# Kernel optimization log

Measured on AMD Instinct MI355X. Metric: run time of the kernel, lower is better.

## Reference

```python
import jax, jax.numpy as jnp
import numpy as np

NEG_BIG = -1e12
ALPHA = 0.2  # leaky_relu negative slope


def setup_inputs() -> dict:
    key = jax.random.key(0)
    k1, k2, k3, k4, k5 = jax.random.split(key, 5)
    B, N, C_in, C_out = 8, 2048, 128, 128
    x = jax.random.normal(k1, (B, N, C_in), dtype=jnp.float32)
    adj = jax.random.randint(k2, (B, N, N), 0, 2, dtype=jnp.int32)
    W = jax.random.normal(k3, (C_in, C_out), dtype=jnp.float32)
    a = jax.random.normal(k4, (C_out, 2), dtype=jnp.float32)
    bias = jax.random.normal(k5, (C_out,), dtype=jnp.float32)
    return {"x": x, "adj": adj, "W": W, "a": a, "bias": bias}


def reference(x, adj, W, a, bias):
    # hidden: [B, N, C_out]
    hidden = jnp.matmul(x, W)
    # additive attention components: [B, N, 2] -> attn1, attn2 each [B, N]
    scores = jnp.matmul(hidden, a)
    attn1 = scores[..., 0]
    attn2 = scores[..., 1]
    # outer-sum: [B, N, N]
    attn = attn1[:, :, None] + attn2[:, None, :]
    attn = jnp.where(attn >= 0, attn, ALPHA * attn)  # leaky_relu
    attn = attn + jnp.where(adj > 0, 0.0, NEG_BIG)
    attn = jax.nn.softmax(attn, axis=-1)
    # dropout is identity in eval/reference mode
    out = jnp.matmul(attn, hidden) + bias
    return out
```

## Files before the change

kernel.cpp:

```cpp
#include <hip/hip_runtime.h>
#include <hip/hip_bf16.h>

#define ALPHA 0.2f
#define NEG_BIG -1e12f

constexpr int B_ = 8, N_ = 2048, C_ = 128;
constexpr int IB = 16, JB = 128, NJT = N_ / JB;

typedef __attribute__((ext_vector_type(8))) short short8;
typedef __attribute__((ext_vector_type(8))) unsigned short ushort8;
typedef __attribute__((ext_vector_type(4))) float f32x4;

__device__ __forceinline__ unsigned short f2bf(float f) {
    unsigned int u = __float_as_uint(f);
    u += 0x7fffu + ((u >> 16) & 1u);
    return (unsigned short)(u >> 16);
}

__device__ __forceinline__ unsigned int cvtpk_bf16(float lo, float hi) {
    unsigned int r;
    asm("v_cvt_pk_bf16_f32 %0, %1, %2" : "=v"(r) : "v"(lo), "v"(hi));
    return r;
}

__device__ __forceinline__ void barrier_lds_only() {
    asm volatile("s_waitcnt lgkmcnt(0)" ::: "memory");
    __builtin_amdgcn_s_barrier();
}

__global__ __launch_bounds__(256) void k1_hidden(
    const float* __restrict__ x, const float* __restrict__ W,
    const float* __restrict__ a, unsigned short* __restrict__ hT,
    float* __restrict__ at1, float* __restrict__ at2)
{
    __shared__ float xs[64][C_];
    __shared__ float Ws[C_][C_];
    const int tid = threadIdx.x;
    const int row0 = blockIdx.x * 64;

    {
        const float4* xsrc = (const float4*)(x + (size_t)row0 * C_);
        float4* xdst = (float4*)&xs[0][0];
        for (int i = tid; i < 64 * C_ / 4; i += 256) xdst[i] = xsrc[i];
        const float4* wsrc = (const float4*)W;
        float4* wdst = (float4*)&Ws[0][0];
        for (int i = tid; i < C_ * C_ / 4; i += 256) wdst[i] = wsrc[i];
    }
    __syncthreads();

    const int tr = tid >> 5, tc = tid & 31;
    const int r0 = tr * 8, c0 = tc * 4;

    float acc[8][4];
#pragma unroll
    for (int i = 0; i < 8; ++i)
#pragma unroll
        for (int j = 0; j < 4; ++j) acc[i][j] = 0.f;

    for (int k = 0; k < C_; k += 4) {
        float4 w0 = *(const float4*)&Ws[k + 0][c0];
        float4 w1 = *(const float4*)&Ws[k + 1][c0];
        float4 w2 = *(const float4*)&Ws[k + 2][c0];
        float4 w3 = *(const float4*)&Ws[k + 3][c0];
#pragma unroll
        for (int rr = 0; rr < 8; ++rr) {
            float4 xv = *(const float4*)&xs[r0 + rr][k];
            acc[rr][0] += xv.x * w0.x + xv.y * w1.x + xv.z * w2.x + xv.w * w3.x;
            acc[rr][1] += xv.x * w0.y + xv.y * w1.y + xv.z * w2.y + xv.w * w3.y;
            acc[rr][2] += xv.x * w0.z + xv.y * w1.z + xv.z * w2.z + xv.w * w3.z;
            acc[rr][3] += xv.x * w0.w + xv.y * w1.w + xv.z * w2.w + xv.w * w3.w;
        }
    }

    float av0[4], av1[4];
#pragma unroll
    for (int cc = 0; cc < 4; ++cc) {
        av0[cc] = a[(c0 + cc) * 2 + 0];
        av1[cc] = a[(c0 + cc) * 2 + 1];
    }
#pragma unroll
    for (int rr = 0; rr < 8; ++rr) {
        float s1 = acc[rr][0] * av0[0] + acc[rr][1] * av0[1] +
                   acc[rr][2] * av0[2] + acc[rr][3] * av0[3];
        float s2 = acc[rr][0] * av1[0] + acc[rr][1] * av1[1] +
                   acc[rr][2] * av1[2] + acc[rr][3] * av1[3];
#pragma unroll
        for (int off = 1; off < 32; off <<= 1) {
            s1 += __shfl_xor(s1, off);
            s2 += __shfl_xor(s2, off);
        }
        if (tc == 0) {
            at1[row0 + r0 + rr] = s1;
            at2[row0 + r0 + rr] = s2;
        }
    }

    const int b = row0 >> 11;
    const int n0 = row0 & (N_ - 1);
#pragma unroll
    for (int cc = 0; cc < 4; ++cc) {
        ushort8 hv;
#pragma unroll
        for (int rr = 0; rr < 8; ++rr) hv[rr] = f2bf(acc[rr][cc]);
        *(ushort8*)(hT + ((size_t)b * C_ + c0 + cc) * N_ + n0 + r0) = hv;
    }
}

__global__ __launch_bounds__(256, 4) void k2_attn(
    const int* __restrict__ adj, const unsigned short* __restrict__ hT,
    const float* __restrict__ at1, const float* __restrict__ at2,
    const float* __restrict__ bias, float* __restrict__ out)
{
    __shared__ unsigned short P[2][IB][JB + 8];
    __shared__ float at2s[N_];
    __shared__ float mrow[IB], lrow[IB], srow[2][IB];

    const int tid = threadIdx.x;
    const int b  = blockIdx.x >> 7;
    const int i0 = (blockIdx.x & 127) * IB;

    {
        const float4* src = (const float4*)(at2 + (size_t)b * N_);
        float4* dst = (float4*)at2s;
        dst[tid]       = src[tid];
        dst[tid + 256] = src[tid + 256];
    }
    if (tid < IB) { mrow[tid] = -3e38f; lrow[tid] = 0.f; }

    const int r  = tid >> 4;
    const int jl = tid & 15;
    const float a1 = at1[(size_t)b * N_ + i0 + r];
    const int* arow = adj + ((size_t)(b * N_ + i0 + r)) * N_ + jl * 8;

    const int lane = tid & 63;
    const int wv = tid >> 6;
    const int lg = lane >> 4;
    const int ll = lane & 15;
    const unsigned short* hb = hT + ((size_t)b * C_ + wv * 32 + ll) * N_;

    f32x4 acc0 = {0.f, 0.f, 0.f, 0.f}, acc1 = {0.f, 0.f, 0.f, 0.f};

    __syncthreads();

    int4 pf0 = *(const int4*)arow;
    int4 pf1 = *(const int4*)(arow + 4);

    for (int jt = 0; jt < NJT; ++jt) {
        const int buf = jt & 1;

        short8 vb0[4], vb1[4];
        {
            const unsigned short* hrow = hb + jt * JB + lg * 8;
#pragma unroll
            for (int ks = 0; ks < 4; ++ks) {
                vb0[ks] = *(const short8*)(hrow + ks * 32);
                vb1[ks] = *(const short8*)(hrow + (size_t)16 * N_ + ks * 32);
            }
        }

        int4 A0 = pf0, A1 = pf1;
        if (jt + 1 < NJT) {
            pf0 = *(const int4*)(arow + (jt + 1) * JB);
            pf1 = *(const int4*)(arow + (jt + 1) * JB + 4);
        }
        float4 f0 = *(const float4*)&at2s[jt * JB + jl * 8];
        float4 f1 = *(const float4*)&at2s[jt * JB + jl * 8 + 4];

        float s[8];
        {
            float t;
            t = a1 + f0.x; t = fmaxf(t, ALPHA * t); s[0] = A0.x > 0 ? t : NEG_BIG;
            t = a1 + f0.y; t = fmaxf(t, ALPHA * t); s[1] = A0.y > 0 ? t : NEG_BIG;
            t = a1 + f0.z; t = fmaxf(t, ALPHA * t); s[2] = A0.z > 0 ? t : NEG_BIG;
            t = a1 + f0.w; t = fmaxf(t, ALPHA * t); s[3] = A0.w > 0 ? t : NEG_BIG;
            t = a1 + f1.x; t = fmaxf(t, ALPHA * t); s[4] = A1.x > 0 ? t : NEG_BIG;
            t = a1 + f1.y; t = fmaxf(t, ALPHA * t); s[5] = A1.y > 0 ? t : NEG_BIG;
            t = a1 + f1.z; t = fmaxf(t, ALPHA * t); s[6] = A1.z > 0 ? t : NEG_BIG;
            t = a1 + f1.w; t = fmaxf(t, ALPHA * t); s[7] = A1.w > 0 ? t : NEG_BIG;
        }
        float tm = fmaxf(fmaxf(fmaxf(s[0], s[1]), fmaxf(s[2], s[3])),
                         fmaxf(fmaxf(s[4], s[5]), fmaxf(s[6], s[7])));
        tm = fmaxf(tm, __shfl_xor(tm, 1));
        tm = fmaxf(tm, __shfl_xor(tm, 2));
        tm = fmaxf(tm, __shfl_xor(tm, 4));
        tm = fmaxf(tm, __shfl_xor(tm, 8));

        const float m_old = mrow[r];
        const float m_new = fmaxf(m_old, tm);

        float p[8];
        float ps = 0.f;
#pragma unroll
        for (int e = 0; e < 8; ++e) { p[e] = __expf(s[e] - m_new); ps += p[e]; }
        ps += __shfl_xor(ps, 1);
        ps += __shfl_xor(ps, 2);
        ps += __shfl_xor(ps, 4);
        ps += __shfl_xor(ps, 8);

        int4 pw;
        pw.x = (int)cvtpk_bf16(p[0], p[1]);
        pw.y = (int)cvtpk_bf16(p[2], p[3]);
        pw.z = (int)cvtpk_bf16(p[4], p[5]);
        pw.w = (int)cvtpk_bf16(p[6], p[7]);
        *(int4*)&P[buf][r][jl * 8] = pw;

        if (jl == 0) {
            const float sc = __expf(m_old - m_new);
            srow[buf][r] = sc;
            mrow[r] = m_new;
            lrow[r] = lrow[r] * sc + ps;
        }
        barrier_lds_only();

        const char* Pb = (const char*)P[buf];
        short8 pa[4];
#pragma unroll
        for (int ks = 0; ks < 4; ++ks)
            pa[ks] = *(const short8*)(Pb + ll * 272 + ks * 64 + lg * 16);

        float4 sc4 = *(const float4*)&srow[buf][lg * 4];
        acc0[0] *= sc4.x; acc0[1] *= sc4.y; acc0[2] *= sc4.z; acc0[3] *= sc4.w;
        acc1[0] *= sc4.x; acc1[1] *= sc4.y; acc1[2] *= sc4.z; acc1[3] *= sc4.w;

        __builtin_amdgcn_s_setprio(1);
#pragma unroll
        for (int ks = 0; ks < 4; ++ks) {
            acc0 = __builtin_amdgcn_mfma_f32_16x16x32_bf16(pa[ks], vb0[ks], acc0, 0, 0, 0);
            acc1 = __builtin_amdgcn_mfma_f32_16x16x32_bf16(pa[ks], vb1[ks], acc1, 0, 0, 0);
        }
        __builtin_amdgcn_s_setprio(0);
    }

    float4 lw = *(const float4*)&lrow[lg * 4];
    const int c = wv * 32 + ll;
    const float bv0 = bias[c];
    const float bv1 = bias[c + 16];

    float* o = out + ((size_t)(b * N_ + i0 + lg * 4)) * C_ + c;
    o[0 * C_]      = acc0[0] / lw.x + bv0;
    o[1 * C_]      = acc0[1] / lw.y + bv0;
    o[2 * C_]      = acc0[2] / lw.z + bv0;
    o[3 * C_]      = acc0[3] / lw.w + bv0;
    o[0 * C_ + 16] = acc1[0] / lw.x + bv1;
    o[1 * C_ + 16] = acc1[1] / lw.y + bv1;
    o[2 * C_ + 16] = acc1[2] / lw.z + bv1;
    o[3 * C_ + 16] = acc1[3] / lw.w + bv1;
}

extern "C" void kernel_launch(void* const* d_in, const int* in_sizes, int n_in,
                              void* d_out, int out_size, void* d_ws, size_t ws_size,
                              hipStream_t stream) {
    const float* x    = (const float*)d_in[0];
    const int*   adj  = (const int*)d_in[1];
    const float* W    = (const float*)d_in[2];
    const float* a    = (const float*)d_in[3];
    const float* bias = (const float*)d_in[4];
    float* out = (float*)d_out;

    char* ws = (char*)d_ws;
    unsigned short* hT = (unsigned short*)ws;
    float* at1 = (float*)(ws + (size_t)4 * 1024 * 1024);
    float* at2 = (float*)(ws + (size_t)4 * 1024 * 1024 + 64 * 1024);

    k1_hidden<<<(B_ * N_) / 64, 256, 0, stream>>>(x, W, a, hT, at1, at2);
    k2_attn<<<B_ * (N_ / IB), 256, 0, stream>>>(adj, hT, at1, at2, bias, out);
}
```

Before: 86.93 us.

## Compute softmax probabilities in MFMA operand layout to eliminate LDS staging and barriers

The attention kernel is restructured so that each wave computes the 16x128 probability tile itself, already laid out as the MFMA B operand, and multiplies it against transposed hidden tiles as the A operand. The shared P buffer, per-row max/sum arrays and the per-tile barrier go away, and row statistics stay in registers through cross-lane shuffles. Blocks shrink to 128 threads (two waves, each covering 64 output channels) and each thread loads a whole adjacency row tile. Each wave now recomputes the full score and exp work for the tile, so that work is duplicated across waves, and register pressure rises with 32 probabilities and a double-buffered adjacency prefetch.

```diff
diff --git a/kernel.cpp b/kernel.cpp
--- a/kernel.cpp
+++ b/kernel.cpp
@@ -5,7 +5,7 @@
 #define NEG_BIG -1e12f
 
 constexpr int B_ = 8, N_ = 2048, C_ = 128;
-constexpr int IB = 16, JB = 128, NJT = N_ / JB;
+constexpr int JB = 128, NJT = N_ / JB;
 
 typedef __attribute__((ext_vector_type(8))) short short8;
 typedef __attribute__((ext_vector_type(8))) unsigned short ushort8;
@@ -21,11 +21,6 @@
     unsigned int r;
     asm("v_cvt_pk_bf16_f32 %0, %1, %2" : "=v"(r) : "v"(lo), "v"(hi));
     return r;
-}
-
-__device__ __forceinline__ void barrier_lds_only() {
-    asm volatile("s_waitcnt lgkmcnt(0)" ::: "memory");
-    __builtin_amdgcn_s_barrier();
 }
 
 __global__ __launch_bounds__(256) void k1_hidden(
@@ -106,145 +101,151 @@
     }
 }
 
-__global__ __launch_bounds__(256, 4) void k2_attn(
+__global__ __launch_bounds__(128, 2) void k2_attn(
     const int* __restrict__ adj, const unsigned short* __restrict__ hT,
     const float* __restrict__ at1, const float* __restrict__ at2,
     const float* __restrict__ bias, float* __restrict__ out)
 {
-    __shared__ unsigned short P[2][IB][JB + 8];
     __shared__ float at2s[N_];
-    __shared__ float mrow[IB], lrow[IB], srow[2][IB];
-
     const int tid = threadIdx.x;
     const int b  = blockIdx.x >> 7;
-    const int i0 = (blockIdx.x & 127) * IB;
+    const int i0 = (blockIdx.x & 127) * 16;
 
     {
         const float4* src = (const float4*)(at2 + (size_t)b * N_);
         float4* dst = (float4*)at2s;
-        dst[tid]       = src[tid];
-        dst[tid + 256] = src[tid + 256];
-    }
-    if (tid < IB) { mrow[tid] = -3e38f; lrow[tid] = 0.f; }
-
-    const int r  = tid >> 4;
-    const int jl = tid & 15;
-    const float a1 = at1[(size_t)b * N_ + i0 + r];
-    const int* arow = adj + ((size_t)(b * N_ + i0 + r)) * N_ + jl * 8;
+#pragma unroll
+        for (int k = 0; k < 4; ++k) dst[tid + 128 * k] = src[tid + 128 * k];
+    }
 
     const int lane = tid & 63;
     const int wv = tid >> 6;
-    const int lg = lane >> 4;
-    const int ll = lane & 15;
-    const unsigned short* hb = hT + ((size_t)b * C_ + wv * 32 + ll) * N_;
-
-    f32x4 acc0 = {0.f, 0.f, 0.f, 0.f}, acc1 = {0.f, 0.f, 0.f, 0.f};
+    const int r  = lane & 15;
+    const int jc = lane >> 4;
+
+    const float a1v = at1[(size_t)b * N_ + i0 + r];
+    const int* arow = adj + ((size_t)(b * N_ + i0 + r)) * N_ + jc * 8;
+    const unsigned short* hrow = hT + ((size_t)b * C_ + wv * 64 + r) * N_ + jc * 8;
+
+    f32x4 acc[4];
+#pragma unroll
+    for (int cb = 0; cb < 4; ++cb) acc[cb] = (f32x4){0.f, 0.f, 0.f, 0.f};
+    float m = -3e38f, l = 0.f;
+
+    int4 A[8];
+#pragma unroll
+    for (int q = 0; q < 8; ++q)
+        A[q] = *(const int4*)(arow + (q >> 1) * 32 + (q & 1) * 4);
 
     __syncthreads();
 
-    int4 pf0 = *(const int4*)arow;
-    int4 pf1 = *(const int4*)(arow + 4);
-
     for (int jt = 0; jt < NJT; ++jt) {
-        const int buf = jt & 1;
-
-        short8 vb0[4], vb1[4];
-        {
-            const unsigned short* hrow = hb + jt * JB + lg * 8;
-#pragma unroll
-            for (int ks = 0; ks < 4; ++ks) {
-                vb0[ks] = *(const short8*)(hrow + ks * 32);
-                vb1[ks] = *(const short8*)(hrow + (size_t)16 * N_ + ks * 32);
-            }
-        }
-
-        int4 A0 = pf0, A1 = pf1;
-        if (jt + 1 < NJT) {
-            pf0 = *(const int4*)(arow + (jt + 1) * JB);
-            pf1 = *(const int4*)(arow + (jt + 1) * JB + 4);
-        }
-        float4 f0 = *(const float4*)&at2s[jt * JB + jl * 8];
-        float4 f1 = *(const float4*)&at2s[jt * JB + jl * 8 + 4];
-
-        float s[8];
-        {
+        const int jn = (jt + 1 < NJT ? jt + 1 : jt) * JB;
+        int4 An[8];
+#pragma unroll
+        for (int q = 0; q < 8; ++q)
+            An[q] = *(const int4*)(arow + jn + (q >> 1) * 32 + (q & 1) * 4);
+
+        short8 h0[4], h1[4];
+#pragma unroll
+        for (int ks = 0; ks < 4; ++ks) {
+            h0[ks] = *(const short8*)(hrow + jt * JB + ks * 32);
+            h1[ks] = *(const short8*)(hrow + (size_t)16 * N_ + jt * JB + ks * 32);
+        }
+
+        float4 F[8];
+#pragma unroll
+        for (int q = 0; q < 8; ++q)
+            F[q] = *(const float4*)&at2s[jt * JB + (q >> 1) * 32 + jc * 8 + (q & 1) * 4];
+
+        float p[32];
+#pragma unroll
+        for (int q = 0; q < 8; ++q) {
             float t;
-            t = a1 + f0.x; t = fmaxf(t, ALPHA * t); s[0] = A0.x > 0 ? t : NEG_BIG;
-            t = a1 + f0.y; t = fmaxf(t, ALPHA * t); s[1] = A0.y > 0 ? t : NEG_BIG;
-            t = a1 + f0.z; t = fmaxf(t, ALPHA * t); s[2] = A0.z > 0 ? t : NEG_BIG;
-            t = a1 + f0.w; t = fmaxf(t, ALPHA * t); s[3] = A0.w > 0 ? t : NEG_BIG;
-            t = a1 + f1.x; t = fmaxf(t, ALPHA * t); s[4] = A1.x > 0 ? t : NEG_BIG;
-            t = a1 + f1.y; t = fmaxf(t, ALPHA * t); s[5] = A1.y > 0 ? t : NEG_BIG;
-            t = a1 + f1.z; t = fmaxf(t, ALPHA * t); s[6] = A1.z > 0 ? t : NEG_BIG;
-            t = a1 + f1.w; t = fmaxf(t, ALPHA * t); s[7] = A1.w > 0 ? t : NEG_BIG;
-        }
-        float tm = fmaxf(fmaxf(fmaxf(s[0], s[1]), fmaxf(s[2], s[3])),
-                         fmaxf(fmaxf(s[4], s[5]), fmaxf(s[6], s[7])));
-        tm = fmaxf(tm, __shfl_xor(tm, 1));
-        tm = fmaxf(tm, __shfl_xor(tm, 2));
-        tm = fmaxf(tm, __shfl_xor(tm, 4));
-        tm = fmaxf(tm, __shfl_xor(tm, 8));
-
-        const float m_old = mrow[r];
-        const float m_new = fmaxf(m_old, tm);
-
-        float p[8];
-        float ps = 0.f;
-#pragma unroll
-        for (int e = 0; e < 8; ++e) { p[e] = __expf(s[e] - m_new); ps += p[e]; }
-        ps += __shfl_xor(ps, 1);
-        ps += __shfl_xor(ps, 2);
-        ps += __shfl_xor(ps, 4);
-        ps += __shfl_xor(ps, 8);
-
-        int4 pw;
-        pw.x = (int)cvtpk_bf16(p[0], p[1]);
-        pw.y = (int)cvtpk_bf16(p[2], p[3]);
-        pw.z = (int)cvtpk_bf16(p[4], p[5]);
-        pw.w = (int)cvtpk_bf16(p[6], p[7]);
-        *(int4*)&P[buf][r][jl * 8] = pw;
-
-        if (jl == 0) {
-            const float sc = __expf(m_old - m_new);
-            srow[buf][r] = sc;
-            mrow[r] = m_new;
-            lrow[r] = lrow[r] * sc + ps;
-        }
-        barrier_lds_only();
-
-        const char* Pb = (const char*)P[buf];
-        short8 pa[4];
-#pragma unroll
-        for (int ks = 0; ks < 4; ++ks)
-            pa[ks] = *(const short8*)(Pb + ll * 272 + ks * 64 + lg * 16);
-
-        float4 sc4 = *(const float4*)&srow[buf][lg * 4];
-        acc0[0] *= sc4.x; acc0[1] *= sc4.y; acc0[2] *= sc4.z; acc0[3] *= sc4.w;
-        acc1[0] *= sc4.x; acc1[1] *= sc4.y; acc1[2] *= sc4.z; acc1[3] *= sc4.w;
-
+            t = a1v + F[q].x; t = fmaxf(t, ALPHA * t); p[q * 4 + 0] = A[q].x > 0 ? t : NEG_BIG;
+            t = a1v + F[q].y; t = fmaxf(t, ALPHA * t); p[q * 4 + 1] = A[q].y > 0 ? t : NEG_BIG;
+            t = a1v + F[q].z; t = fmaxf(t, ALPHA * t); p[q * 4 + 2] = A[q].z > 0 ? t : NEG_BIG;
+            t = a1v + F[q].w; t = fmaxf(t, ALPHA * t); p[q * 4 + 3] = A[q].w > 0 ? t : NEG_BIG;
+        }
+
+        short8 h2[4], h3[4];
+#pragma unroll
+        for (int ks = 0; ks < 4; ++ks) {
+            h2[ks] = *(const short8*)(hrow + (size_t)32 * N_ + jt * JB + ks * 32);
+            h3[ks] = *(const short8*)(hrow + (size_t)48 * N_ + jt * JB + ks * 32);
+        }
+
+        float u[16];
+#pragma unroll
+        for (int q = 0; q < 16; ++q) u[q] = fmaxf(p[q], p[q + 16]);
+#pragma unroll
+        for (int q = 0; q < 8; ++q) u[q] = fmaxf(u[q], u[q + 8]);
+#pragma unroll
+        for (int q = 0; q < 4; ++q) u[q] = fmaxf(u[q], u[q + 4]);
+        float tm = fmaxf(fmaxf(u[0], u[1]), fmaxf(u[2], u[3]));
+        tm = fmaxf(tm, __shfl_xor(tm, 16));
+        tm = fmaxf(tm, __shfl_xor(tm, 32));
+
+        const float m_new = fmaxf(m, tm);
+        const float sc = __expf(m - m_new);
+        m = m_new;
+
+#pragma unroll
+        for (int q = 0; q < 32; ++q) p[q] = __expf(p[q] - m_new);
+
+        float v[16];
+#pragma unroll
+        for (int q = 0; q < 16; ++q) v[q] = p[q] + p[q + 16];
+#pragma unroll
+        for (int q = 0; q < 8; ++q) v[q] = v[q] + v[q + 8];
+#pragma unroll
+        for (int q = 0; q < 4; ++q) v[q] = v[q] + v[q + 4];
+        float ps = (v[0] + v[1]) + (v[2] + v[3]);
+        ps += __shfl_xor(ps, 16);
+        ps += __shfl_xor(ps, 32);
+        l = l * sc + ps;
+
+        short8 Pb[4];
+#pragma unroll
+        for (int ks = 0; ks < 4; ++ks) {
+            int4 w;
+            w.x = (int)cvtpk_bf16(p[ks * 8 + 0], p[ks * 8 + 1]);
+            w.y = (int)cvtpk_bf16(p[ks * 8 + 2], p[ks * 8 + 3]);
+            w.z = (int)cvtpk_bf16(p[ks * 8 + 4], p[ks * 8 + 5]);
+            w.w = (int)cvtpk_bf16(p[ks * 8 + 6], p[ks * 8 + 7]);
+            Pb[ks] = *(short8*)&w;
+        }
+
+#pragma unroll
+        for (int cb = 0; cb < 4; ++cb) {
+            acc[cb][0] *= sc; acc[cb][1] *= sc; acc[cb][2] *= sc; acc[cb][3] *= sc;
+        }
         __builtin_amdgcn_s_setprio(1);
 #pragma unroll
         for (int ks = 0; ks < 4; ++ks) {
-            acc0 = __builtin_amdgcn_mfma_f32_16x16x32_bf16(pa[ks], vb0[ks], acc0, 0, 0, 0);
-            acc1 = __builtin_amdgcn_mfma_f32_16x16x32_bf16(pa[ks], vb1[ks], acc1, 0, 0, 0);
+            acc[0] = __builtin_amdgcn_mfma_f32_16x16x32_bf16(h0[ks], Pb[ks], acc[0], 0, 0, 0);
+            acc[1] = __builtin_amdgcn_mfma_f32_16x16x32_bf16(h1[ks], Pb[ks], acc[1], 0, 0, 0);
+            acc[2] = __builtin_amdgcn_mfma_f32_16x16x32_bf16(h2[ks], Pb[ks], acc[2], 0, 0, 0);
+            acc[3] = __builtin_amdgcn_mfma_f32_16x16x32_bf16(h3[ks], Pb[ks], acc[3], 0, 0, 0);
         }
         __builtin_amdgcn_s_setprio(0);
-    }
-
-    float4 lw = *(const float4*)&lrow[lg * 4];
-    const int c = wv * 32 + ll;
-    const float bv0 = bias[c];
-    const float bv1 = bias[c + 16];
-
-    float* o = out + ((size_t)(b * N_ + i0 + lg * 4)) * C_ + c;
-    o[0 * C_]      = acc0[0] / lw.x + bv0;
-    o[1 * C_]      = acc0[1] / lw.y + bv0;
-    o[2 * C_]      = acc0[2] / lw.z + bv0;
-    o[3 * C_]      = acc0[3] / lw.w + bv0;
-    o[0 * C_ + 16] = acc1[0] / lw.x + bv1;
-    o[1 * C_ + 16] = acc1[1] / lw.y + bv1;
-    o[2 * C_ + 16] = acc1[2] / lw.z + bv1;
-    o[3 * C_ + 16] = acc1[3] / lw.w + bv1;
+
+#pragma unroll
+        for (int q = 0; q < 8; ++q) A[q] = An[q];
+    }
+
+    const float invl = 1.f / l;
+#pragma unroll
+    for (int cb = 0; cb < 4; ++cb) {
+        const int c0 = wv * 64 + cb * 16 + jc * 4;
+        float4 bv = *(const float4*)&bias[c0];
+        float4 o;
+        o.x = acc[cb][0] * invl + bv.x;
+        o.y = acc[cb][1] * invl + bv.y;
+        o.z = acc[cb][2] * invl + bv.z;
+        o.w = acc[cb][3] * invl + bv.w;
+        *(float4*)(out + ((size_t)(b * N_ + i0 + r)) * C_ + c0) = o;
+    }
 }
 
 extern "C" void kernel_launch(void* const* d_in, const int* in_sizes, int n_in,
@@ -263,5 +264,5 @@
     float* at2 = (float*)(ws + (size_t)4 * 1024 * 1024 + 64 * 1024);
 
     k1_hidden<<<(B_ * N_) / 64, 256, 0, stream>>>(x, W, a, hT, at1, at2);
-    k2_attn<<<B_ * (N_ / IB), 256, 0, stream>>>(adj, hT, at1, at2, bias, out);
-}
+    k2_attn<<<B_ * (N_ / 16), 128, 0, stream>>>(adj, hT, at1, at2, bias, out);
+}
```

After: 113.0 us, median of 4. 1.3x slower.

## Pre-pack adjacency into bitmask and use exp2 with log2e-scaled scores

Applied to the files above, without the earlier changes.

Adds a streaming kernel that compresses the int32 adjacency matrix into one bit per entry, so the attention kernel reads a small bitmask instead of full int32 rows inside its softmax loop. The attention scores are pre-scaled by log2(e) in the hidden kernel so the softmax can use exp2 instead of exp. The full adjacency is still read once, but now by a simple bandwidth-oriented kernel. The cost is an extra launch and extra workspace writes, and the new 4 MB workspace region shifts the other buffers.

```diff
diff --git a/kernel.cpp b/kernel.cpp
--- a/kernel.cpp
+++ b/kernel.cpp
@@ -3,6 +3,7 @@
 
 #define ALPHA 0.2f
 #define NEG_BIG -1e12f
+#define LOG2E 1.44269504088896340736f
 
 constexpr int B_ = 8, N_ = 2048, C_ = 128;
 constexpr int IB = 16, JB = 128, NJT = N_ / JB;
@@ -26,6 +27,25 @@
 __device__ __forceinline__ void barrier_lds_only() {
     asm volatile("s_waitcnt lgkmcnt(0)" ::: "memory");
     __builtin_amdgcn_s_barrier();
+}
+
+__global__ __launch_bounds__(256) void k_pack(
+    const int* __restrict__ adj, unsigned int* __restrict__ abits)
+{
+    const size_t w = (size_t)blockIdx.x * 256 + threadIdx.x;
+    const int4* src = (const int4*)adj + w * 8;
+    int4 v[8];
+#pragma unroll
+    for (int q = 0; q < 8; ++q) v[q] = src[q];
+    unsigned int m = 0;
+#pragma unroll
+    for (int q = 0; q < 8; ++q) {
+        m |= (v[q].x > 0 ? 1u : 0u) << (q * 4 + 0);
+        m |= (v[q].y > 0 ? 1u : 0u) << (q * 4 + 1);
+        m |= (v[q].z > 0 ? 1u : 0u) << (q * 4 + 2);
+        m |= (v[q].w > 0 ? 1u : 0u) << (q * 4 + 3);
+    }
+    abits[w] = m;
 }
 
 __global__ __launch_bounds__(256) void k1_hidden(
@@ -90,8 +110,8 @@
             s2 += __shfl_xor(s2, off);
         }
         if (tc == 0) {
-            at1[row0 + r0 + rr] = s1;
-            at2[row0 + r0 + rr] = s2;
+            at1[row0 + r0 + rr] = s1 * LOG2E;
+            at2[row0 + r0 + rr] = s2 * LOG2E;
         }
     }
 
@@ -107,7 +127,7 @@
 }
 
 __global__ __launch_bounds__(256, 4) void k2_attn(
-    const int* __restrict__ adj, const unsigned short* __restrict__ hT,
+    const unsigned int* __restrict__ abits, const unsigned short* __restrict__ hT,
     const float* __restrict__ at1, const float* __restrict__ at2,
     const float* __restrict__ bias, float* __restrict__ out)
 {
@@ -129,8 +149,10 @@
 
     const int r  = tid >> 4;
     const int jl = tid & 15;
-    const float a1 = at1[(size_t)b * N_ + i0 + r];
-    const int* arow = adj + ((size_t)(b * N_ + i0 + r)) * N_ + jl * 8;
+    const float a1v = at1[(size_t)b * N_ + i0 + r];
+    const unsigned int* abrow =
+        abits + ((size_t)(b * N_ + i0 + r)) * (N_ / 32) + (jl >> 2);
+    const int sh = (jl & 3) * 8;
 
     const int lane = tid & 63;
     const int wv = tid >> 6;
@@ -142,11 +164,10 @@
 
     __syncthreads();
 
-    int4 pf0 = *(const int4*)arow;
-    int4 pf1 = *(const int4*)(arow + 4);
-
     for (int jt = 0; jt < NJT; ++jt) {
         const int buf = jt & 1;
+
+        const unsigned int wbits = abrow[jt * 4] >> sh;
 
         short8 vb0[4], vb1[4];
         {
@@ -158,25 +179,20 @@
             }
         }
 
-        int4 A0 = pf0, A1 = pf1;
-        if (jt + 1 < NJT) {
-            pf0 = *(const int4*)(arow + (jt + 1) * JB);
-            pf1 = *(const int4*)(arow + (jt + 1) * JB + 4);
-        }
         float4 f0 = *(const float4*)&at2s[jt * JB + jl * 8];
         float4 f1 = *(const float4*)&at2s[jt * JB + jl * 8 + 4];
 
         float s[8];
         {
             float t;
-            t = a1 + f0.x; t = fmaxf(t, ALPHA * t); s[0] = A0.x > 0 ? t : NEG_BIG;
-            t = a1 + f0.y; t = fmaxf(t, ALPHA * t); s[1] = A0.y > 0 ? t : NEG_BIG;
-            t = a1 + f0.z; t = fmaxf(t, ALPHA * t); s[2] = A0.z > 0 ? t : NEG_BIG;
-            t = a1 + f0.w; t = fmaxf(t, ALPHA * t); s[3] = A0.w > 0 ? t : NEG_BIG;
-            t = a1 + f1.x; t = fmaxf(t, ALPHA * t); s[4] = A1.x > 0 ? t : NEG_BIG;
-            t = a1 + f1.y; t = fmaxf(t, ALPHA * t); s[5] = A1.y > 0 ? t : NEG_BIG;
-            t = a1 + f1.z; t = fmaxf(t, ALPHA * t); s[6] = A1.z > 0 ? t : NEG_BIG;
-            t = a1 + f1.w; t = fmaxf(t, ALPHA * t); s[7] = A1.w > 0 ? t : NEG_BIG;
+            t = a1v + f0.x; t = fmaxf(t, ALPHA * t); s[0] = (wbits & 1u)   ? t : NEG_BIG;
+            t = a1v + f0.y; t = fmaxf(t, ALPHA * t); s[1] = (wbits & 2u)   ? t : NEG_BIG;
+            t = a1v + f0.z; t = fmaxf(t, ALPHA * t); s[2] = (wbits & 4u)   ? t : NEG_BIG;
+            t = a1v + f0.w; t = fmaxf(t, ALPHA * t); s[3] = (wbits & 8u)   ? t : NEG_BIG;
+            t = a1v + f1.x; t = fmaxf(t, ALPHA * t); s[4] = (wbits & 16u)  ? t : NEG_BIG;
+            t = a1v + f1.y; t = fmaxf(t, ALPHA * t); s[5] = (wbits & 32u)  ? t : NEG_BIG;
+            t = a1v + f1.z; t = fmaxf(t, ALPHA * t); s[6] = (wbits & 64u)  ? t : NEG_BIG;
+            t = a1v + f1.w; t = fmaxf(t, ALPHA * t); s[7] = (wbits & 128u) ? t : NEG_BIG;
         }
         float tm = fmaxf(fmaxf(fmaxf(s[0], s[1]), fmaxf(s[2], s[3])),
                          fmaxf(fmaxf(s[4], s[5]), fmaxf(s[6], s[7])));
@@ -191,7 +207,7 @@
         float p[8];
         float ps = 0.f;
 #pragma unroll
-        for (int e = 0; e < 8; ++e) { p[e] = __expf(s[e] - m_new); ps += p[e]; }
+        for (int e = 0; e < 8; ++e) { p[e] = exp2f(s[e] - m_new); ps += p[e]; }
         ps += __shfl_xor(ps, 1);
         ps += __shfl_xor(ps, 2);
         ps += __shfl_xor(ps, 4);
@@ -205,7 +221,7 @@
         *(int4*)&P[buf][r][jl * 8] = pw;
 
         if (jl == 0) {
-            const float sc = __expf(m_old - m_new);
+            const float sc = exp2f(m_old - m_new);
             srow[buf][r] = sc;
             mrow[r] = m_new;
             lrow[r] = lrow[r] * sc + ps;
@@ -258,10 +274,12 @@
     float* out = (float*)d_out;
 
     char* ws = (char*)d_ws;
-    unsigned short* hT = (unsigned short*)ws;
-    float* at1 = (float*)(ws + (size_t)4 * 1024 * 1024);
-    float* at2 = (float*)(ws + (size_t)4 * 1024 * 1024 + 64 * 1024);
-
+    unsigned int*   abits = (unsigned int*)ws;
+    unsigned short* hT  = (unsigned short*)(ws + (size_t)4 * 1024 * 1024);
+    float* at1 = (float*)(ws + (size_t)8 * 1024 * 1024);
+    float* at2 = (float*)(ws + (size_t)8 * 1024 * 1024 + 64 * 1024);
+
+    k_pack<<<(B_ * N_ * (N_ / 32)) / 256, 256, 0, stream>>>(adj, abits);
     k1_hidden<<<(B_ * N_) / 64, 256, 0, stream>>>(x, W, a, hT, at1, at2);
-    k2_attn<<<B_ * (N_ / IB), 256, 0, stream>>>(adj, hT, at1, at2, bias, out);
-}
+    k2_attn<<<B_ * (N_ / IB), 256, 0, stream>>>(abits, hT, at1, at2, bias, out);
+}
```

After: 106.6 us. 22.6% more time.

## Double attention row block to 32 rows and use exp2 with prescaled scores

Applied to the files above, without the earlier changes.

The attention kernel now handles 32 query rows per block with 512 threads, so two row-halves of waves share the same hT column tiles and at2 staging. This halves redundant loads of the bf16 hidden matrix per output row. The attention scores are also prescaled by log2(e) in the first kernel so the softmax can use exp2 instead of exp. In exchange the grid has half as many blocks, which may reduce load balance across CUs.

```diff
diff --git a/kernel.cpp b/kernel.cpp
--- a/kernel.cpp
+++ b/kernel.cpp
@@ -3,9 +3,10 @@
 
 #define ALPHA 0.2f
 #define NEG_BIG -1e12f
+#define LOG2E 1.44269504088896340736f
 
 constexpr int B_ = 8, N_ = 2048, C_ = 128;
-constexpr int IB = 16, JB = 128, NJT = N_ / JB;
+constexpr int IB = 32, JB = 128, NJT = N_ / JB;
 
 typedef __attribute__((ext_vector_type(8))) short short8;
 typedef __attribute__((ext_vector_type(8))) unsigned short ushort8;
@@ -90,8 +91,8 @@
             s2 += __shfl_xor(s2, off);
         }
         if (tc == 0) {
-            at1[row0 + r0 + rr] = s1;
-            at2[row0 + r0 + rr] = s2;
+            at1[row0 + r0 + rr] = s1 * LOG2E;
+            at2[row0 + r0 + rr] = s2 * LOG2E;
         }
     }
 
@@ -106,7 +107,7 @@
     }
 }
 
-__global__ __launch_bounds__(256, 4) void k2_attn(
+__global__ __launch_bounds__(512, 2) void k2_attn(
     const int* __restrict__ adj, const unsigned short* __restrict__ hT,
     const float* __restrict__ at1, const float* __restrict__ at2,
     const float* __restrict__ bias, float* __restrict__ out)
@@ -116,24 +117,21 @@
     __shared__ float mrow[IB], lrow[IB], srow[2][IB];
 
     const int tid = threadIdx.x;
-    const int b  = blockIdx.x >> 7;
-    const int i0 = (blockIdx.x & 127) * IB;
-
-    {
-        const float4* src = (const float4*)(at2 + (size_t)b * N_);
-        float4* dst = (float4*)at2s;
-        dst[tid]       = src[tid];
-        dst[tid + 256] = src[tid + 256];
-    }
+    const int b  = blockIdx.x >> 6;
+    const int i0 = (blockIdx.x & 63) * IB;
+
+    ((float4*)at2s)[tid] = ((const float4*)(at2 + (size_t)b * N_))[tid];
     if (tid < IB) { mrow[tid] = -3e38f; lrow[tid] = 0.f; }
 
     const int r  = tid >> 4;
     const int jl = tid & 15;
-    const float a1 = at1[(size_t)b * N_ + i0 + r];
+    const float a1v = at1[(size_t)b * N_ + i0 + r];
     const int* arow = adj + ((size_t)(b * N_ + i0 + r)) * N_ + jl * 8;
 
     const int lane = tid & 63;
-    const int wv = tid >> 6;
+    const int w  = tid >> 6;
+    const int wv = w & 3;
+    const int rh = w >> 2;
     const int lg = lane >> 4;
     const int ll = lane & 15;
     const unsigned short* hb = hT + ((size_t)b * C_ + wv * 32 + ll) * N_;
@@ -169,14 +167,14 @@
         float s[8];
         {
             float t;
-            t = a1 + f0.x; t = fmaxf(t, ALPHA * t); s[0] = A0.x > 0 ? t : NEG_BIG;
-            t = a1 + f0.y; t = fmaxf(t, ALPHA * t); s[1] = A0.y > 0 ? t : NEG_BIG;
-            t = a1 + f0.z; t = fmaxf(t, ALPHA * t); s[2] = A0.z > 0 ? t : NEG_BIG;
-            t = a1 + f0.w; t = fmaxf(t, ALPHA * t); s[3] = A0.w > 0 ? t : NEG_BIG;
-            t = a1 + f1.x; t = fmaxf(t, ALPHA * t); s[4] = A1.x > 0 ? t : NEG_BIG;
-            t = a1 + f1.y; t = fmaxf(t, ALPHA * t); s[5] = A1.y > 0 ? t : NEG_BIG;
-            t = a1 + f1.z; t = fmaxf(t, ALPHA * t); s[6] = A1.z > 0 ? t : NEG_BIG;
-            t = a1 + f1.w; t = fmaxf(t, ALPHA * t); s[7] = A1.w > 0 ? t : NEG_BIG;
+            t = a1v + f0.x; t = fmaxf(t, ALPHA * t); s[0] = A0.x > 0 ? t : NEG_BIG;
+            t = a1v + f0.y; t = fmaxf(t, ALPHA * t); s[1] = A0.y > 0 ? t : NEG_BIG;
+            t = a1v + f0.z; t = fmaxf(t, ALPHA * t); s[2] = A0.z > 0 ? t : NEG_BIG;
+            t = a1v + f0.w; t = fmaxf(t, ALPHA * t); s[3] = A0.w > 0 ? t : NEG_BIG;
+            t = a1v + f1.x; t = fmaxf(t, ALPHA * t); s[4] = A1.x > 0 ? t : NEG_BIG;
+            t = a1v + f1.y; t = fmaxf(t, ALPHA * t); s[5] = A1.y > 0 ? t : NEG_BIG;
+            t = a1v + f1.z; t = fmaxf(t, ALPHA * t); s[6] = A1.z > 0 ? t : NEG_BIG;
+            t = a1v + f1.w; t = fmaxf(t, ALPHA * t); s[7] = A1.w > 0 ? t : NEG_BIG;
         }
         float tm = fmaxf(fmaxf(fmaxf(s[0], s[1]), fmaxf(s[2], s[3])),
                          fmaxf(fmaxf(s[4], s[5]), fmaxf(s[6], s[7])));
@@ -191,7 +189,7 @@
         float p[8];
         float ps = 0.f;
 #pragma unroll
-        for (int e = 0; e < 8; ++e) { p[e] = __expf(s[e] - m_new); ps += p[e]; }
+        for (int e = 0; e < 8; ++e) { p[e] = exp2f(s[e] - m_new); ps += p[e]; }
         ps += __shfl_xor(ps, 1);
         ps += __shfl_xor(ps, 2);
         ps += __shfl_xor(ps, 4);
@@ -205,7 +203,7 @@
         *(int4*)&P[buf][r][jl * 8] = pw;
 
         if (jl == 0) {
-            const float sc = __expf(m_old - m_new);
+            const float sc = exp2f(m_old - m_new);
             srow[buf][r] = sc;
             mrow[r] = m_new;
             lrow[r] = lrow[r] * sc + ps;
@@ -216,9 +214,9 @@
         short8 pa[4];
 #pragma unroll
         for (int ks = 0; ks < 4; ++ks)
-            pa[ks] = *(const short8*)(Pb + ll * 272 + ks * 64 + lg * 16);
-
-        float4 sc4 = *(const float4*)&srow[buf][lg * 4];
+            pa[ks] = *(const short8*)(Pb + (rh * 16 + ll) * 272 + ks * 64 + lg * 16);
+
+        float4 sc4 = *(const float4*)&srow[buf][rh * 16 + lg * 4];
         acc0[0] *= sc4.x; acc0[1] *= sc4.y; acc0[2] *= sc4.z; acc0[3] *= sc4.w;
         acc1[0] *= sc4.x; acc1[1] *= sc4.y; acc1[2] *= sc4.z; acc1[3] *= sc4.w;
 
@@ -231,12 +229,12 @@
         __builtin_amdgcn_s_setprio(0);
     }
 
-    float4 lw = *(const float4*)&lrow[lg * 4];
+    float4 lw = *(const float4*)&lrow[rh * 16 + lg * 4];
     const int c = wv * 32 + ll;
     const float bv0 = bias[c];
     const float bv1 = bias[c + 16];
 
-    float* o = out + ((size_t)(b * N_ + i0 + lg * 4)) * C_ + c;
+    float* o = out + ((size_t)(b * N_ + i0 + rh * 16 + lg * 4)) * C_ + c;
     o[0 * C_]      = acc0[0] / lw.x + bv0;
     o[1 * C_]      = acc0[1] / lw.y + bv0;
     o[2 * C_]      = acc0[2] / lw.z + bv0;
@@ -263,5 +261,5 @@
     float* at2 = (float*)(ws + (size_t)4 * 1024 * 1024 + 64 * 1024);
 
     k1_hidden<<<(B_ * N_) / 64, 256, 0, stream>>>(x, W, a, hT, at1, at2);
-    k2_attn<<<B_ * (N_ / IB), 256, 0, stream>>>(adj, hT, at1, at2, bias, out);
-}
+    k2_attn<<<B_ * (N_ / IB), 512, 0, stream>>>(adj, hT, at1, at2, bias, out);
+}
```

Result: slower. 89.19 us (+2.6%).
